# Optimization experiments

Hardware: AMD Instinct MI355X
Metric: run time of the kernel (lower is better)

Reference implementation:

```python
import jax, jax.numpy as jnp
import numpy as np

HEADS = 8
HEAD_DIM = 64
FOLD = 2   # fold_w == fold_h
PROP = 2   # proposal_w == proposal_h -> M = PROP*PROP centers
DIM = 512


def _conv1x1(x, w, b):
    # x: [B,C,H,W], w: [O,C] (1x1 conv kernel squeezed), b: [O]
    return jnp.einsum('bchw,oc->bohw', x, w) + b[None, :, None, None]


def _normalize(x):
    # F.normalize along last dim (eps-clamped L2 norm)
    n = jnp.linalg.norm(x, axis=-1, keepdims=True)
    return x / jnp.maximum(n, 1e-12)


def _fold(t, f):
    # 'b c (f1 w) (f2 h) -> (b f1 f2) c w h'
    b, c, W, H = t.shape
    return t.reshape(b, c, f, W // f, f, H // f).transpose(0, 2, 4, 1, 3, 5).reshape(b * f * f, c, W // f, H // f)


def _unfold(t, f):
    # '(b f1 f2) c w h -> b c (f1 w) (f2 h)'
    bf, c, w, h = t.shape
    b = bf // (f * f)
    return t.reshape(b, f, f, c, w, h).transpose(0, 3, 1, 4, 2, 5).reshape(b, c, f * w, f * h)


def _pool(t, p):
    # AdaptiveAvgPool2d((p,p)) when spatial dims divisible by p
    b, c, W, H = t.shape
    return t.reshape(b, c, p, W // p, p, H // p).mean(axis=(3, 5))


def reference(x, f_w, f_b, v_w, v_b, proj_w, proj_b, sim_alpha, sim_beta):
    B = x.shape[0]
    value = _conv1x1(x, v_w, v_b)
    feat = _conv1x1(x, f_w, f_b)
    # split heads: 'b (e c) w h -> (b e) c w h'
    feat = feat.reshape(B * HEADS, HEAD_DIM, feat.shape[2], feat.shape[3])
    value = value.reshape(B * HEADS, HEAD_DIM, value.shape[2], value.shape[3])
    feat = _fold(feat, FOLD)
    value = _fold(value, FOLD)
    b, c, w, h = feat.shape

    centers = _pool(feat, PROP)                                   # [b,c,p,p]
    value_centers = _pool(value, PROP).reshape(b, c, -1).transpose(0, 2, 1)  # [b,M,c]
    cflat = centers.reshape(b, c, -1).transpose(0, 2, 1)          # [b,M,c]
    M = cflat.shape[1]
    xflat = feat.reshape(b, c, -1).transpose(0, 2, 1)             # [b,N,c]

    cos = jnp.einsum('bmc,bnc->bmn', _normalize(cflat), _normalize(xflat))
    sim = jax.nn.sigmoid(sim_beta + sim_alpha * cos)              # [b,M,N]

    idx = jnp.argmax(sim, axis=1)                                 # [b,N] hard assignment
    sim_max = jnp.max(sim, axis=1)
    L_Clst = -jnp.mean(sim_max)
    mask = jax.nn.one_hot(idx, M, dtype=sim.dtype).transpose(0, 2, 1)  # [b,M,N]
    L_Sep = jnp.mean(jnp.max(sim * (1.0 - mask), axis=1))
    Cn = _normalize(cflat)
    G = jnp.einsum('bmc,bkc->bmk', Cn, Cn)
    L_Orth = jnp.mean((G - jnp.eye(M, dtype=G.dtype)) ** 2)

    sim_m = sim * mask
    vflat = value.reshape(b, c, -1).transpose(0, 2, 1)            # [b,N,c]
    # scatter_sum of values into their assigned cluster == one-hot matmul
    agg = jnp.einsum('bmn,bnc->bmc', mask, vflat)                 # [b,M,c]
    counts = mask.sum(axis=-1, keepdims=True)                     # [b,M,1]
    out = (agg + value_centers) / (counts + 1.0)                  # [b,M,c]
    # masked weighted broadcast back to points (avoids [b,M,N,c] intermediate)
    outp = jnp.einsum('bmn,bmc->bnc', sim_m, out)                 # [b,N,c]
    outp = outp.transpose(0, 2, 1).reshape(b, c, w, h)
    outp = _unfold(outp, FOLD)
    outp = outp.reshape(B, HEADS * HEAD_DIM, outp.shape[2], outp.shape[3])
    outp = _conv1x1(outp, proj_w, proj_b)
    return outp, jnp.stack([L_Orth, L_Clst, L_Sep])


def setup_inputs():
    key = jax.random.key(0)
    ks = jax.random.split(key, 4)
    E = HEADS * HEAD_DIM  # 512
    return {
        'x': jax.random.normal(ks[0], (32, DIM, 32, 32), jnp.float32),
        'f_w': jax.random.normal(ks[1], (E, DIM), jnp.float32) * 0.02,
        'f_b': jnp.zeros((E,), jnp.float32),
        'v_w': jax.random.normal(ks[2], (E, DIM), jnp.float32) * 0.02,
        'v_b': jnp.zeros((E,), jnp.float32),
        'proj_w': jax.random.normal(ks[3], (DIM, E), jnp.float32) * 0.02,
        'proj_b': jnp.zeros((DIM,), jnp.float32),
        'sim_alpha': jnp.ones((1,), jnp.float32),
        'sim_beta': jnp.zeros((1,), jnp.float32),
    }
```

## Files before the change

### kernel.cpp

```cpp
#include <hip/hip_runtime.h>


#define HW 1024

typedef _Float16 f16x8 __attribute__((ext_vector_type(8)));
typedef float f32x4 __attribute__((ext_vector_type(4)));

union H4 { uint2 u; _Float16 h[4]; };
union H8 { uint4 u; _Float16 h[8]; };
union H2 { unsigned int u; _Float16 h[2]; };
union F4 { float4 v; float f[4]; };

__device__ __forceinline__ void gld16(const _Float16* g, _Float16* l) {
    __builtin_amdgcn_global_load_lds(
        (const __attribute__((address_space(1))) void*)g,
        (__attribute__((address_space(3))) void*)l, 16, 0, 0);
}

__global__ __launch_bounds__(256) void k_wsplit(
    const float* __restrict__ fw, const float* __restrict__ vw,
    _Float16* __restrict__ fwh, _Float16* __restrict__ fwl,
    _Float16* __restrict__ vwh)
{
    const int i = (blockIdx.x * 256 + threadIdx.x) * 4;
    F4 a;
    a.v = *(const float4*)&fw[i];
    H4 h, l;
#pragma unroll
    for (int j = 0; j < 4; ++j) {
        const float s = a.f[j] * 256.f;
        h.h[j] = (_Float16)s;
        l.h[j] = (_Float16)(s - (float)h.h[j]);
    }
    *(uint2*)&fwh[i] = h.u;
    *(uint2*)&fwl[i] = l.u;
    a.v = *(const float4*)&vw[i];
#pragma unroll
    for (int j = 0; j < 4; ++j) h.h[j] = (_Float16)(a.f[j] * 256.f);
    *(uint2*)&vwh[i] = h.u;
}

__global__ __launch_bounds__(256) void k_xsplit(
    const float* __restrict__ x,
    _Float16* __restrict__ xh, _Float16* __restrict__ xl)
{
    __shared__ float tile[64][65];
    const int t = threadIdx.x;
    const int b = blockIdx.z;
    const int k0 = blockIdx.y * 64;
    const int n0 = blockIdx.x * 64;
    const float* Xb = x + (size_t)b * (512 * HW);

#pragma unroll
    for (int j = 0; j < 16; ++j) {
        const int k = j * 4 + (t >> 6);
        const int n = t & 63;
        tile[k][n] = Xb[(size_t)(k0 + k) * HW + n0 + n];
    }
    __syncthreads();
#pragma unroll
    for (int j = 0; j < 8; ++j) {
        const int n = j * 8 + (t >> 5);
        const int kp = t & 31;
        const float s0 = tile[kp * 2][n] * 256.f;
        const float s1 = tile[kp * 2 + 1][n] * 256.f;
        H2 hh, hl;
        hh.h[0] = (_Float16)s0;
        hh.h[1] = (_Float16)s1;
        hl.h[0] = (_Float16)(s0 - (float)hh.h[0]);
        hl.h[1] = (_Float16)(s1 - (float)hh.h[1]);
        const size_t o = ((size_t)b * 1024 + n0 + n) * 512 + k0 + kp * 2;
        *(unsigned int*)&xh[o] = hh.u;
        *(unsigned int*)&xl[o] = hl.u;
    }
}

__global__ __launch_bounds__(512, 2) void k_featval(
    const _Float16* __restrict__ fwh, const _Float16* __restrict__ fwl,
    const _Float16* __restrict__ vwh,
    const float* __restrict__ f_b, const float* __restrict__ v_b,
    const _Float16* __restrict__ xh, const _Float16* __restrict__ xl,
    float* __restrict__ feat_T, float* __restrict__ centers_f,
    _Float16* __restrict__ value_T, float* __restrict__ centers_v)
{
    __shared__ _Float16 Ah[2][8192], Al[2][8192], Bh[2][8192], Bl[2][8192];
    __shared__ float pool_lds[4][4][256];
    const int t = threadIdx.x, lane = t & 63, wv = t >> 6;
    const int b = blockIdx.z, o0 = blockIdx.y * 256, p0 = blockIdx.x * 256;
    const int wr = wv >> 2, wc = wv & 3;

    f32x4 acc[8][4];
#pragma unroll
    for (int i = 0; i < 8; ++i)
#pragma unroll
        for (int j = 0; j < 4; ++j) acc[i][j] = (f32x4){0.f, 0.f, 0.f, 0.f};

    const int gslot = ((lane & 3) ^ ((lane >> 3) & 3)) * 8;
    const _Float16* ash = fwh + (size_t)(o0 + wv * 32 + (lane >> 2)) * 512 + gslot;
    const _Float16* asl = fwl + (size_t)(o0 + wv * 32 + (lane >> 2)) * 512 + gslot;
    const _Float16* asv = vwh + (size_t)(o0 + wv * 32 + (lane >> 2)) * 512 + gslot;
    const size_t brow = (size_t)b * 1024 + p0 + wv * 32 + (lane >> 2);
    const _Float16* bsh = xh + brow * 512 + gslot;
    const _Float16* bsl = xl + brow * 512 + gslot;

#define STAGE_F(d, k0)                                              \
    {                                                               \
        gld16(ash + (k0),        &Ah[(d)][(wv * 32) * 32]);         \
        gld16(ash + (k0) + 8192, &Ah[(d)][(wv * 32 + 16) * 32]);    \
        gld16(asl + (k0),        &Al[(d)][(wv * 32) * 32]);         \
        gld16(asl + (k0) + 8192, &Al[(d)][(wv * 32 + 16) * 32]);    \
        gld16(bsh + (k0),        &Bh[(d)][(wv * 32) * 32]);         \
        gld16(bsh + (k0) + 8192, &Bh[(d)][(wv * 32 + 16) * 32]);    \
        gld16(bsl + (k0),        &Bl[(d)][(wv * 32) * 32]);         \
        gld16(bsl + (k0) + 8192, &Bl[(d)][(wv * 32 + 16) * 32]);    \
    }
#define STAGE_W(d, k0)                                              \
    {                                                               \
        gld16(asv + (k0),        &Ah[(d)][(wv * 32) * 32]);         \
        gld16(asv + (k0) + 8192, &Ah[(d)][(wv * 32 + 16) * 32]);    \
        gld16(bsh + (k0),        &Bh[(d)][(wv * 32) * 32]);         \
        gld16(bsh + (k0) + 8192, &Bh[(d)][(wv * 32 + 16) * 32]);    \
    }

    STAGE_F(0, 0);
    const int slA = ((lane >> 4) ^ ((lane >> 1) & 3)) * 8;
    int cur = 0;
    for (int kb = 0; kb < 16; ++kb) {
        if (kb < 15) {
            STAGE_F(cur ^ 1, (kb + 1) * 32);
            asm volatile("s_waitcnt vmcnt(8)" ::: "memory");
        } else {
            asm volatile("s_waitcnt vmcnt(0)" ::: "memory");
        }
        __builtin_amdgcn_sched_barrier(0);
        __builtin_amdgcn_s_barrier();
        f16x8 bh4[4], bl4[4];
#pragma unroll
        for (int j = 0; j < 4; ++j) {
            const int bo = (wc * 64 + j * 16 + (lane & 15)) * 32 + slA;
            bh4[j] = *(f16x8*)&Bh[cur][bo];
            bl4[j] = *(f16x8*)&Bl[cur][bo];
        }
#pragma unroll
        for (int mi = 0; mi < 8; ++mi) {
            const int ao = (wr * 128 + mi * 16 + (lane & 15)) * 32 + slA;
            const f16x8 ah = *(f16x8*)&Ah[cur][ao];
            const f16x8 al = *(f16x8*)&Al[cur][ao];
#pragma unroll
            for (int nj = 0; nj < 4; ++nj) {
                acc[mi][nj] = __builtin_amdgcn_mfma_f32_16x16x32_f16(ah, bh4[nj], acc[mi][nj], 0, 0, 0);
                acc[mi][nj] = __builtin_amdgcn_mfma_f32_16x16x32_f16(ah, bl4[nj], acc[mi][nj], 0, 0, 0);
                acc[mi][nj] = __builtin_amdgcn_mfma_f32_16x16x32_f16(al, bh4[nj], acc[mi][nj], 0, 0, 0);
            }
        }
        __builtin_amdgcn_s_barrier();
        cur ^= 1;
    }

    STAGE_W(0, 0);

    const int pj = (lane >> 3) & 1;
    {
        float ps[32][2];
#pragma unroll
        for (int mi = 0; mi < 8; ++mi) {
            const int obase = o0 + wr * 128 + mi * 16 + (lane >> 4) * 4;
            F4 bs4;
            bs4.v = *(const float4*)&f_b[obase];
#pragma unroll
            for (int r = 0; r < 4; ++r) { ps[mi * 4 + r][0] = 0.f; ps[mi * 4 + r][1] = 0.f; }
#pragma unroll
            for (int nj = 0; nj < 4; ++nj) {
                const int p = p0 + wc * 64 + nj * 16 + (lane & 15);
                F4 vv;
#pragma unroll
                for (int r = 0; r < 4; ++r) {
                    vv.f[r] = acc[mi][nj][r] * (1.f / 65536.f) + bs4.f[r];
                    ps[mi * 4 + r][nj & 1] += vv.f[r];
                }
                *(float4*)&feat_T[((size_t)b * 1024 + p) * 512 + obase] = vv.v;
            }
        }
#pragma unroll
        for (int q = 0; q < 32; ++q)
#pragma unroll
            for (int f2s = 0; f2s < 2; ++f2s) {
                ps[q][f2s] += __shfl_xor(ps[q][f2s], 1);
                ps[q][f2s] += __shfl_xor(ps[q][f2s], 2);
                ps[q][f2s] += __shfl_xor(ps[q][f2s], 4);
            }
        if ((lane & 7) == 0) {
#pragma unroll
            for (int mi = 0; mi < 8; ++mi)
#pragma unroll
                for (int r = 0; r < 4; ++r) {
                    const int ol = wr * 128 + mi * 16 + (lane >> 4) * 4 + r;
                    pool_lds[wc][0 * 2 + pj][ol] = ps[mi * 4 + r][0];
                    pool_lds[wc][1 * 2 + pj][ol] = ps[mi * 4 + r][1];
                }
        }
        __syncthreads();
#pragma unroll
        for (int u = 0; u < 2; ++u) {
            const int idx = u * 512 + t;
            const int g = idx >> 8, o = idx & 255;
            const float s = pool_lds[0][g][o] + pool_lds[1][g][o]
                          + pool_lds[2][g][o] + pool_lds[3][g][o];
            centers_f[(((size_t)b * 8 + 2 * blockIdx.x) * 4 + g) * 512 + o0 + o] = s;
            centers_f[(((size_t)b * 8 + 2 * blockIdx.x + 1) * 4 + g) * 512 + o0 + o] = 0.f;
        }
    }

    f32x4 vacc[8][4];
#pragma unroll
    for (int i = 0; i < 8; ++i)
#pragma unroll
        for (int j = 0; j < 4; ++j) vacc[i][j] = (f32x4){0.f, 0.f, 0.f, 0.f};

    cur = 0;
    for (int kb = 0; kb < 16; ++kb) {
        if (kb < 15) {
            STAGE_W(cur ^ 1, (kb + 1) * 32);
            asm volatile("s_waitcnt vmcnt(4)" ::: "memory");
        } else {
            asm volatile("s_waitcnt vmcnt(0)" ::: "memory");
        }
        __builtin_amdgcn_sched_barrier(0);
        __builtin_amdgcn_s_barrier();
        f16x8 bh4[4];
#pragma unroll
        for (int j = 0; j < 4; ++j)
            bh4[j] = *(f16x8*)&Bh[cur][(wc * 64 + j * 16 + (lane & 15)) * 32 + slA];
#pragma unroll
        for (int mi = 0; mi < 8; ++mi) {
            const f16x8 ah = *(f16x8*)&Ah[cur][(wr * 128 + mi * 16 + (lane & 15)) * 32 + slA];
#pragma unroll
            for (int nj = 0; nj < 4; ++nj)
                vacc[mi][nj] = __builtin_amdgcn_mfma_f32_16x16x32_f16(ah, bh4[nj], vacc[mi][nj], 0, 0, 0);
        }
        __builtin_amdgcn_s_barrier();
        cur ^= 1;
    }
#undef STAGE_F
#undef STAGE_W

    {
        float ps[32][2];
#pragma unroll
        for (int mi = 0; mi < 8; ++mi) {
            const int obase = o0 + wr * 128 + mi * 16 + (lane >> 4) * 4;
            F4 bs4;
            bs4.v = *(const float4*)&v_b[obase];
#pragma unroll
            for (int r = 0; r < 4; ++r) { ps[mi * 4 + r][0] = 0.f; ps[mi * 4 + r][1] = 0.f; }
#pragma unroll
            for (int nj = 0; nj < 4; ++nj) {
                const int p = p0 + wc * 64 + nj * 16 + (lane & 15);
                H4 hv;
#pragma unroll
                for (int r = 0; r < 4; ++r) {
                    const float v = vacc[mi][nj][r] * (1.f / 65536.f) + bs4.f[r];
                    ps[mi * 4 + r][nj & 1] += v;
                    hv.h[r] = (_Float16)v;
                }
                *(uint2*)&value_T[((size_t)b * 1024 + p) * 512 + obase] = hv.u;
            }
        }
#pragma unroll
        for (int q = 0; q < 32; ++q)
#pragma unroll
            for (int f2s = 0; f2s < 2; ++f2s) {
                ps[q][f2s] += __shfl_xor(ps[q][f2s], 1);
                ps[q][f2s] += __shfl_xor(ps[q][f2s], 2);
                ps[q][f2s] += __shfl_xor(ps[q][f2s], 4);
            }
        __syncthreads();
        if ((lane & 7) == 0) {
#pragma unroll
            for (int mi = 0; mi < 8; ++mi)
#pragma unroll
                for (int r = 0; r < 4; ++r) {
                    const int ol = wr * 128 + mi * 16 + (lane >> 4) * 4 + r;
                    pool_lds[wc][0 * 2 + pj][ol] = ps[mi * 4 + r][0];
                    pool_lds[wc][1 * 2 + pj][ol] = ps[mi * 4 + r][1];
                }
        }
        __syncthreads();
#pragma unroll
        for (int u = 0; u < 2; ++u) {
            const int idx = u * 512 + t;
            const int g = idx >> 8, o = idx & 255;
            const float s = pool_lds[0][g][o] + pool_lds[1][g][o]
                          + pool_lds[2][g][o] + pool_lds[3][g][o];
            centers_v[(((size_t)b * 8 + 2 * blockIdx.x) * 4 + g) * 512 + o0 + o] = s;
            centers_v[(((size_t)b * 8 + 2 * blockIdx.x + 1) * 4 + g) * 512 + o0 + o] = 0.f;
        }
    }
}

__global__ __launch_bounds__(256) void k_cluster(
    const float* __restrict__ feat_T, const _Float16* __restrict__ value_T,
    const float* __restrict__ centers_f, const float* __restrict__ centers_v,
    const float* __restrict__ alpha_p, const float* __restrict__ beta_p,
    _Float16* __restrict__ outpT, float* __restrict__ part)
{
    __shared__ float cnl[4][64];
    __shared__ float vcl[4][64];
    __shared__ float obuf[4][68];
    __shared__ int   sidx[256];
    __shared__ float sbest[256];
    __shared__ float scrt[4][4][64];
    __shared__ int   cntw[4][4];
    __shared__ float red[8];
    __shared__ float gsc[16];

    const int t = threadIdx.x, lane = t & 63, wv = t >> 6;
    const int bp = blockIdx.x;
    const int f2 = bp & 1, f1 = (bp >> 1) & 1, head = (bp >> 2) & 7, b = bp >> 5;

    const int m = wv, cc = lane;
    const int pi = m >> 1, pj = m & 1, g = f2 * 2 + pj;
    const int pt = 4 * f1 + 2 * pi;
    {
        const float* cf = centers_f + (((size_t)b * 8 + pt) * 4 + g) * 512 + head * 64 + cc;
        const float c = (cf[0] + cf[4 * 512]) * (1.f / 64.f);
        float ss = c * c;
#pragma unroll
        for (int off = 32; off > 0; off >>= 1) ss += __shfl_xor(ss, off);
        const float inv = 1.f / fmaxf(sqrtf(ss), 1e-12f);
        cnl[m][cc] = c * inv;
        const float* cv = centers_v + (((size_t)b * 8 + pt) * 4 + g) * 512 + head * 64 + cc;
        vcl[m][cc] = (cv[0] + cv[4 * 512]) * (1.f / 64.f);
    }
    __syncthreads();

    if (t < 16) {
        const int gm = t >> 2, gk = t & 3;
        float gg = 0.f;
        for (int c = 0; c < 64; ++c) gg += cnl[gm][c] * cnl[gk][c];
        const float d = gg - (gm == gk ? 1.f : 0.f);
        gsc[t] = d * d;
    }

    const float alpha = alpha_p[0], beta = beta_p[0];
    const int n = t;
    const int pg = (f1 * 16 + (n >> 4)) * 32 + f2 * 16 + (n & 15);
    const float* fp = feat_T + ((size_t)b * 1024 + pg) * 512 + head * 64;
    float ssf = 0.f, d0 = 0.f, d1 = 0.f, d2 = 0.f, d3 = 0.f;
#pragma unroll
    for (int c4 = 0; c4 < 16; ++c4) {
        F4 fv;
        fv.v = *(const float4*)&fp[c4 * 4];
        const float4 c0 = *(const float4*)&cnl[0][c4 * 4];
        const float4 c1 = *(const float4*)&cnl[1][c4 * 4];
        const float4 c2 = *(const float4*)&cnl[2][c4 * 4];
        const float4 c3 = *(const float4*)&cnl[3][c4 * 4];
        ssf += fv.f[0]*fv.f[0] + fv.f[1]*fv.f[1] + fv.f[2]*fv.f[2] + fv.f[3]*fv.f[3];
        d0 += fv.f[0]*c0.x + fv.f[1]*c0.y + fv.f[2]*c0.z + fv.f[3]*c0.w;
        d1 += fv.f[0]*c1.x + fv.f[1]*c1.y + fv.f[2]*c1.z + fv.f[3]*c1.w;
        d2 += fv.f[0]*c2.x + fv.f[1]*c2.y + fv.f[2]*c2.z + fv.f[3]*c2.w;
        d3 += fv.f[0]*c3.x + fv.f[1]*c3.y + fv.f[2]*c3.z + fv.f[3]*c3.w;
    }
    const float invf = 1.f / fmaxf(sqrtf(ssf), 1e-12f);
    float simv[4];
    simv[0] = d0 * invf;
    simv[1] = d1 * invf;
    simv[2] = d2 * invf;
    simv[3] = d3 * invf;
#pragma unroll
    for (int mm = 0; mm < 4; ++mm)
        simv[mm] = 1.f / (1.f + expf(-(beta + alpha * simv[mm])));
    float best = simv[0], second = -1.f;
    int idx = 0;
#pragma unroll
    for (int mm = 1; mm < 4; ++mm) {
        if (simv[mm] > best) { second = best; best = simv[mm]; idx = mm; }
        else second = fmaxf(second, simv[mm]);
    }
    sidx[n] = idx;
    sbest[n] = best;

    float bsum = best, s2sum = second;
#pragma unroll
    for (int off = 32; off > 0; off >>= 1) {
        bsum += __shfl_xor(bsum, off);
        s2sum += __shfl_xor(s2sum, off);
    }
    if (lane == 0) { red[wv] = bsum; red[4 + wv] = s2sum; }
    __syncthreads();
    if (t == 0) {
        part[bp]        = gsc[0] + gsc[1] + gsc[2] + gsc[3] + gsc[4] + gsc[5] + gsc[6] + gsc[7]
                        + gsc[8] + gsc[9] + gsc[10] + gsc[11] + gsc[12] + gsc[13] + gsc[14] + gsc[15];
        part[1024 + bp] = red[0] + red[1] + red[2] + red[3];
        part[2048 + bp] = red[4] + red[5] + red[6] + red[7];
    }

    {
        const _Float16* vT = value_T + ((size_t)b * 1024) * 512 + head * 64 + cc;
        const int rowbase = (f1 * 16 + wv * 4) * 32 + f2 * 16;
        float ag0 = 0.f, ag1 = 0.f, ag2 = 0.f, ag3 = 0.f;
        int c0i = 0, c1i = 0, c2i = 0, c3i = 0;
#pragma unroll 8
        for (int j = 0; j < 64; ++j) {
            const int nn = wv * 64 + j;
            const int id = sidx[nn];
            const int pgn = rowbase + (j >> 4) * 32 + (j & 15);
            const float v = (float)vT[(size_t)pgn * 512];
            ag0 += (id == 0) ? v : 0.f;  c0i += (id == 0);
            ag1 += (id == 1) ? v : 0.f;  c1i += (id == 1);
            ag2 += (id == 2) ? v : 0.f;  c2i += (id == 2);
            ag3 += (id == 3) ? v : 0.f;  c3i += (id == 3);
        }
        scrt[wv][0][cc] = ag0;
        scrt[wv][1][cc] = ag1;
        scrt[wv][2][cc] = ag2;
        scrt[wv][3][cc] = ag3;
        if (lane == 0) {
            cntw[wv][0] = c0i; cntw[wv][1] = c1i;
            cntw[wv][2] = c2i; cntw[wv][3] = c3i;
        }
    }
    __syncthreads();

    {
        const float a = scrt[0][m][cc] + scrt[1][m][cc] + scrt[2][m][cc] + scrt[3][m][cc];
        const int c = cntw[0][m] + cntw[1][m] + cntw[2][m] + cntw[3][m];
        obuf[m][cc] = (a + vcl[m][cc]) / (float)(c + 1);
    }
    __syncthreads();

    const int cch = (t & 3) * 16;
#pragma unroll
    for (int r = 0; r < 4; ++r) {
        const int nn = r * 64 + (t >> 2);
        const int id = sidx[nn];
        const float bs = sbest[nn];
        const int p = (f1 * 16 + (nn >> 4)) * 32 + f2 * 16 + (nn & 15);
        _Float16* dst = outpT + (((size_t)b * 8 + head) * 1024 + p) * 64 + cch;
        const float4 oa = *(const float4*)&obuf[id][cch];
        const float4 ob = *(const float4*)&obuf[id][cch + 4];
        const float4 oc = *(const float4*)&obuf[id][cch + 8];
        const float4 od = *(const float4*)&obuf[id][cch + 12];
        H8 w0, w1;
        w0.h[0] = (_Float16)(bs * oa.x); w0.h[1] = (_Float16)(bs * oa.y);
        w0.h[2] = (_Float16)(bs * oa.z); w0.h[3] = (_Float16)(bs * oa.w);
        w0.h[4] = (_Float16)(bs * ob.x); w0.h[5] = (_Float16)(bs * ob.y);
        w0.h[6] = (_Float16)(bs * ob.z); w0.h[7] = (_Float16)(bs * ob.w);
        w1.h[0] = (_Float16)(bs * oc.x); w1.h[1] = (_Float16)(bs * oc.y);
        w1.h[2] = (_Float16)(bs * oc.z); w1.h[3] = (_Float16)(bs * oc.w);
        w1.h[4] = (_Float16)(bs * od.x); w1.h[5] = (_Float16)(bs * od.y);
        w1.h[6] = (_Float16)(bs * od.z); w1.h[7] = (_Float16)(bs * od.w);
        *(uint4*)dst = w0.u;
        *(uint4*)(dst + 8) = w1.u;
    }
}

__global__ __launch_bounds__(256) void k_proj(
    const float* __restrict__ w, const float* __restrict__ bias,
    const _Float16* __restrict__ outpT,
    const float* __restrict__ part,
    float* __restrict__ dout)
{
    __shared__ _Float16 As[2][4096], Bs[2][4096];
    __shared__ float fin[12];
    const int t = threadIdx.x, lane = t & 63, wv = t >> 6;

    if (blockIdx.x == 0 && blockIdx.y == 0 && blockIdx.z == 0) {
        float so = part[t] + part[t + 256] + part[t + 512] + part[t + 768];
        float sc = part[1024 + t] + part[1280 + t] + part[1536 + t] + part[1792 + t];
        float sp = part[2048 + t] + part[2304 + t] + part[2560 + t] + part[2816 + t];
#pragma unroll
        for (int off = 32; off > 0; off >>= 1) {
            so += __shfl_xor(so, off);
            sc += __shfl_xor(sc, off);
            sp += __shfl_xor(sp, off);
        }
        if (lane == 0) { fin[wv] = so; fin[4 + wv] = sc; fin[8 + wv] = sp; }
        __syncthreads();
        if (t == 0) {
            dout[16777216]     = (fin[0] + fin[1] + fin[2] + fin[3]) / 16384.f;
            dout[16777216 + 1] = -(fin[4] + fin[5] + fin[6] + fin[7]) / 262144.f;
            dout[16777216 + 2] = (fin[8] + fin[9] + fin[10] + fin[11]) / 262144.f;
        }
        __syncthreads();
    }

    const int b = blockIdx.z, o0 = blockIdx.y * 128, p0 = blockIdx.x * 128;
    const int wr = wv >> 1, wc = wv & 1;

    f32x4 acc[4][4];
#pragma unroll
    for (int i = 0; i < 4; ++i)
#pragma unroll
        for (int j = 0; j < 4; ++j) acc[i][j] = (f32x4){0.f, 0.f, 0.f, 0.f};

    const int gslot = ((lane & 3) ^ ((lane >> 3) & 3)) * 8;
    const int srow = p0 + wv * 32 + (lane >> 2);
    const int arow_l = t >> 3;
    const int aq = t & 7;
    const int aqs = aq ^ (((t >> 4) & 3) << 1);

    F4 av[4];
#define LOADA(k0)                                                        \
    {                                                                    \
        _Pragma("unroll")                                                \
        for (int j = 0; j < 4; ++j)                                      \
            av[j].v = *(const float4*)&w[(size_t)(o0 + j * 32 + arow_l) * 512 + (k0) + aq * 4]; \
    }
#define WRITEA(d)                                                        \
    {                                                                    \
        _Pragma("unroll")                                                \
        for (int j = 0; j < 4; ++j) {                                    \
            H4 hh;                                                       \
            _Pragma("unroll")                                            \
            for (int i = 0; i < 4; ++i) hh.h[i] = (_Float16)(av[j].f[i] * 256.f); \
            *(uint2*)&As[(d)][(j * 32 + arow_l) * 32 + aqs * 4] = hh.u;  \
        }                                                                \
    }
#define STAGEB(d, kb)                                                    \
    {                                                                    \
        const _Float16* bsrc = outpT + (((size_t)b * 8 + ((kb) >> 1)) * 1024 + srow) * 64 \
                               + ((kb) & 1) * 32 + gslot;                \
        gld16(bsrc,        &Bs[(d)][(wv * 32) * 32]);                    \
        gld16(bsrc + 1024, &Bs[(d)][(wv * 32 + 16) * 32]);               \
    }

    LOADA(0);
    STAGEB(0, 0);
    WRITEA(0);
    __syncthreads();
    const int slA = ((lane >> 4) ^ ((lane >> 1) & 3)) * 8;
    int cur = 0;
    for (int kb = 0; kb < 16; ++kb) {
        if (kb < 15) {
            LOADA((kb + 1) * 32);
            STAGEB(cur ^ 1, kb + 1);
        }
        f16x8 ah4[4], bh4[4];
#pragma unroll
        for (int i = 0; i < 4; ++i) {
            ah4[i] = *(f16x8*)&As[cur][(wr * 64 + i * 16 + (lane & 15)) * 32 + slA];
            bh4[i] = *(f16x8*)&Bs[cur][(wc * 64 + i * 16 + (lane & 15)) * 32 + slA];
        }
#pragma unroll
        for (int mi = 0; mi < 4; ++mi)
#pragma unroll
            for (int nj = 0; nj < 4; ++nj)
                acc[mi][nj] = __builtin_amdgcn_mfma_f32_16x16x32_f16(ah4[mi], bh4[nj], acc[mi][nj], 0, 0, 0);
        if (kb < 15) WRITEA(cur ^ 1);
        __syncthreads();
        cur ^= 1;
    }
#undef LOADA
#undef WRITEA
#undef STAGEB

#pragma unroll
    for (int mi = 0; mi < 4; ++mi)
#pragma unroll
        for (int r = 0; r < 4; ++r) {
            const int o = o0 + wr * 64 + mi * 16 + (lane >> 4) * 4 + r;
            const float bs = bias[o];
#pragma unroll
            for (int nj = 0; nj < 4; ++nj) {
                const int p = p0 + wc * 64 + nj * 16 + (lane & 15);
                dout[((size_t)b * 512 + o) * HW + p] = acc[mi][nj][r] * (1.f / 256.f) + bs;
            }
        }
}

extern "C" void kernel_launch(void* const* d_in, const int* in_sizes, int n_in,
                              void* d_out, int out_size, void* d_ws, size_t ws_size,
                              hipStream_t stream)
{
    const float* x   = (const float*)d_in[0];
    const float* f_w = (const float*)d_in[1];
    const float* f_b = (const float*)d_in[2];
    const float* v_w = (const float*)d_in[3];
    const float* v_b = (const float*)d_in[4];
    const float* p_w = (const float*)d_in[5];
    const float* p_b = (const float*)d_in[6];
    const float* s_a = (const float*)d_in[7];
    const float* s_b = (const float*)d_in[8];
    float* out = (float*)d_out;

    char* ws = (char*)d_ws;
    float*     feat_T  = (float*)ws;
    _Float16*  xh      = (_Float16*)(ws + (size_t)64 * 1024 * 1024);
    _Float16*  xl      = (_Float16*)(ws + (size_t)96 * 1024 * 1024);
    _Float16*  outpT   = xh;
    _Float16*  value_T = xl;
    float*     part    = (float*)(ws + (size_t)128 * 1024 * 1024);

    _Float16* fwh       = (_Float16*)out;
    _Float16* fwl       = (_Float16*)(out + 131072);
    _Float16* vwh       = (_Float16*)(out + 262144);
    float*    centers_f = out + 524288;
    float*    centers_v = out + 1048576;

    k_wsplit <<<dim3(256), 256, 0, stream>>>(f_w, v_w, fwh, fwl, vwh);
    k_xsplit <<<dim3(16, 8, 32), 256, 0, stream>>>(x, xh, xl);
    k_featval<<<dim3(4, 2, 32), 512, 0, stream>>>(fwh, fwl, vwh, f_b, v_b, xh, xl,
                                                  feat_T, centers_f, value_T, centers_v);
    k_cluster<<<dim3(1024), 256, 0, stream>>>(feat_T, value_T, centers_f, centers_v,
                                              s_a, s_b, outpT, part);
    k_proj   <<<dim3(8, 4, 32), 256, 0, stream>>>(p_w, p_b, outpT, part, out);
}
```

Before: 186.0 us.

## Fold weight split into x-split kernel and enlarge proj tile to 256x256

Removes the separate weight-split launch by having batch-0 blocks of the x-split kernel also convert f_w/v_w to fp16 hi/lo. The projection GEMM moves from 128x128 tiles with 4 waves to 256x256 tiles with 8 waves. This gives more operand reuse per LDS load, with A fragments loaded per row-tile inside the MFMA loop. __syncthreads is replaced by explicit vmcnt/lgkmcnt waits and s_barrier so global loads overlap compute. Larger tiles cut the grid to 256 blocks and raise register/LDS pressure, and the hand-written wait counts risk races if miscounted.

```diff
diff --git a/kernel.cpp b/kernel.cpp
--- a/kernel.cpp
+++ b/kernel.cpp
@@ -17,40 +17,43 @@
         (__attribute__((address_space(3))) void*)l, 16, 0, 0);
 }
 
-__global__ __launch_bounds__(256) void k_wsplit(
+__global__ __launch_bounds__(256) void k_xsplit(
+    const float* __restrict__ x,
+    _Float16* __restrict__ xh, _Float16* __restrict__ xl,
     const float* __restrict__ fw, const float* __restrict__ vw,
     _Float16* __restrict__ fwh, _Float16* __restrict__ fwl,
     _Float16* __restrict__ vwh)
-{
-    const int i = (blockIdx.x * 256 + threadIdx.x) * 4;
-    F4 a;
-    a.v = *(const float4*)&fw[i];
-    H4 h, l;
-#pragma unroll
-    for (int j = 0; j < 4; ++j) {
-        const float s = a.f[j] * 256.f;
-        h.h[j] = (_Float16)s;
-        l.h[j] = (_Float16)(s - (float)h.h[j]);
-    }
-    *(uint2*)&fwh[i] = h.u;
-    *(uint2*)&fwl[i] = l.u;
-    a.v = *(const float4*)&vw[i];
-#pragma unroll
-    for (int j = 0; j < 4; ++j) h.h[j] = (_Float16)(a.f[j] * 256.f);
-    *(uint2*)&vwh[i] = h.u;
-}
-
-__global__ __launch_bounds__(256) void k_xsplit(
-    const float* __restrict__ x,
-    _Float16* __restrict__ xh, _Float16* __restrict__ xl)
 {
     __shared__ float tile[64][65];
     const int t = threadIdx.x;
     const int b = blockIdx.z;
     const int k0 = blockIdx.y * 64;
     const int n0 = blockIdx.x * 64;
+
+    if (b == 0) {
+        const int c0 = (blockIdx.x * 8 + blockIdx.y) * 2;
+#pragma unroll
+        for (int u = 0; u < 2; ++u) {
+            const int i = ((c0 + u) * 256 + t) * 4;
+            F4 a;
+            a.v = *(const float4*)&fw[i];
+            H4 h, l;
+#pragma unroll
+            for (int j = 0; j < 4; ++j) {
+                const float s = a.f[j] * 256.f;
+                h.h[j] = (_Float16)s;
+                l.h[j] = (_Float16)(s - (float)h.h[j]);
+            }
+            *(uint2*)&fwh[i] = h.u;
+            *(uint2*)&fwl[i] = l.u;
+            a.v = *(const float4*)&vw[i];
+#pragma unroll
+            for (int j = 0; j < 4; ++j) h.h[j] = (_Float16)(a.f[j] * 256.f);
+            *(uint2*)&vwh[i] = h.u;
+        }
+    }
+
     const float* Xb = x + (size_t)b * (512 * HW);
-
 #pragma unroll
     for (int j = 0; j < 16; ++j) {
         const int k = j * 4 + (t >> 6);
@@ -455,48 +458,51 @@
     }
 }
 
-__global__ __launch_bounds__(256) void k_proj(
+__global__ __launch_bounds__(512, 2) void k_proj(
     const float* __restrict__ w, const float* __restrict__ bias,
     const _Float16* __restrict__ outpT,
     const float* __restrict__ part,
     float* __restrict__ dout)
 {
-    __shared__ _Float16 As[2][4096], Bs[2][4096];
-    __shared__ float fin[12];
+    __shared__ _Float16 As[2][8192], Bs[2][8192];
+    __shared__ float fin[24];
     const int t = threadIdx.x, lane = t & 63, wv = t >> 6;
 
     if (blockIdx.x == 0 && blockIdx.y == 0 && blockIdx.z == 0) {
-        float so = part[t] + part[t + 256] + part[t + 512] + part[t + 768];
-        float sc = part[1024 + t] + part[1280 + t] + part[1536 + t] + part[1792 + t];
-        float sp = part[2048 + t] + part[2304 + t] + part[2560 + t] + part[2816 + t];
+        float so = part[t] + part[t + 512];
+        float sc = part[1024 + t] + part[1536 + t];
+        float sp = part[2048 + t] + part[2560 + t];
 #pragma unroll
         for (int off = 32; off > 0; off >>= 1) {
             so += __shfl_xor(so, off);
             sc += __shfl_xor(sc, off);
             sp += __shfl_xor(sp, off);
         }
-        if (lane == 0) { fin[wv] = so; fin[4 + wv] = sc; fin[8 + wv] = sp; }
+        if (lane == 0) { fin[wv] = so; fin[8 + wv] = sc; fin[16 + wv] = sp; }
         __syncthreads();
         if (t == 0) {
-            dout[16777216]     = (fin[0] + fin[1] + fin[2] + fin[3]) / 16384.f;
-            dout[16777216 + 1] = -(fin[4] + fin[5] + fin[6] + fin[7]) / 262144.f;
-            dout[16777216 + 2] = (fin[8] + fin[9] + fin[10] + fin[11]) / 262144.f;
+            float a = 0.f, bsum = 0.f, c = 0.f;
+#pragma unroll
+            for (int i = 0; i < 8; ++i) { a += fin[i]; bsum += fin[8 + i]; c += fin[16 + i]; }
+            dout[16777216]     = a / 16384.f;
+            dout[16777216 + 1] = -bsum / 262144.f;
+            dout[16777216 + 2] = c / 262144.f;
         }
         __syncthreads();
     }
 
-    const int b = blockIdx.z, o0 = blockIdx.y * 128, p0 = blockIdx.x * 128;
-    const int wr = wv >> 1, wc = wv & 1;
-
-    f32x4 acc[4][4];
-#pragma unroll
-    for (int i = 0; i < 4; ++i)
+    const int b = blockIdx.z, o0 = blockIdx.y * 256, p0 = blockIdx.x * 256;
+    const int wr = wv >> 2, wc = wv & 3;
+
+    f32x4 acc[8][4];
+#pragma unroll
+    for (int i = 0; i < 8; ++i)
 #pragma unroll
         for (int j = 0; j < 4; ++j) acc[i][j] = (f32x4){0.f, 0.f, 0.f, 0.f};
 
     const int gslot = ((lane & 3) ^ ((lane >> 3) & 3)) * 8;
     const int srow = p0 + wv * 32 + (lane >> 2);
-    const int arow_l = t >> 3;
+    const int arow = t >> 3;
     const int aq = t & 7;
     const int aqs = aq ^ (((t >> 4) & 3) << 1);
 
@@ -505,7 +511,7 @@
     {                                                                    \
         _Pragma("unroll")                                                \
         for (int j = 0; j < 4; ++j)                                      \
-            av[j].v = *(const float4*)&w[(size_t)(o0 + j * 32 + arow_l) * 512 + (k0) + aq * 4]; \
+            av[j].v = *(const float4*)&w[(size_t)(o0 + j * 64 + arow) * 512 + (k0) + aq * 4]; \
     }
 #define WRITEA(d)                                                        \
     {                                                                    \
@@ -514,7 +520,7 @@
             H4 hh;                                                       \
             _Pragma("unroll")                                            \
             for (int i = 0; i < 4; ++i) hh.h[i] = (_Float16)(av[j].f[i] * 256.f); \
-            *(uint2*)&As[(d)][(j * 32 + arow_l) * 32 + aqs * 4] = hh.u;  \
+            *(uint2*)&As[(d)][(j * 64 + arow) * 32 + aqs * 4] = hh.u;    \
         }                                                                \
     }
 #define STAGEB(d, kb)                                                    \
@@ -528,27 +534,37 @@
     LOADA(0);
     STAGEB(0, 0);
     WRITEA(0);
-    __syncthreads();
+    asm volatile("s_waitcnt lgkmcnt(0)" ::: "memory");
     const int slA = ((lane >> 4) ^ ((lane >> 1) & 3)) * 8;
     int cur = 0;
     for (int kb = 0; kb < 16; ++kb) {
         if (kb < 15) {
             LOADA((kb + 1) * 32);
             STAGEB(cur ^ 1, kb + 1);
-        }
-        f16x8 ah4[4], bh4[4];
-#pragma unroll
-        for (int i = 0; i < 4; ++i) {
-            ah4[i] = *(f16x8*)&As[cur][(wr * 64 + i * 16 + (lane & 15)) * 32 + slA];
-            bh4[i] = *(f16x8*)&Bs[cur][(wc * 64 + i * 16 + (lane & 15)) * 32 + slA];
-        }
-#pragma unroll
-        for (int mi = 0; mi < 4; ++mi)
+            asm volatile("s_waitcnt vmcnt(6)" ::: "memory");
+        } else {
+            asm volatile("s_waitcnt vmcnt(0)" ::: "memory");
+        }
+        __builtin_amdgcn_sched_barrier(0);
+        __builtin_amdgcn_s_barrier();
+        f16x8 bh4[4];
+#pragma unroll
+        for (int j = 0; j < 4; ++j)
+            bh4[j] = *(f16x8*)&Bs[cur][(wc * 64 + j * 16 + (lane & 15)) * 32 + slA];
+#pragma unroll
+        for (int mi = 0; mi < 8; ++mi) {
+            const f16x8 ah = *(f16x8*)&As[cur][(wr * 128 + mi * 16 + (lane & 15)) * 32 + slA];
 #pragma unroll
             for (int nj = 0; nj < 4; ++nj)
-                acc[mi][nj] = __builtin_amdgcn_mfma_f32_16x16x32_f16(ah4[mi], bh4[nj], acc[mi][nj], 0, 0, 0);
-        if (kb < 15) WRITEA(cur ^ 1);
-        __syncthreads();
+                acc[mi][nj] = __builtin_amdgcn_mfma_f32_16x16x32_f16(ah, bh4[nj], acc[mi][nj], 0, 0, 0);
+        }
+        if (kb < 15) {
+            asm volatile("s_waitcnt vmcnt(2)" ::: "memory");
+            __builtin_amdgcn_sched_barrier(0);
+            WRITEA(cur ^ 1);
+        }
+        asm volatile("s_waitcnt lgkmcnt(0)" ::: "memory");
+        __builtin_amdgcn_s_barrier();
         cur ^= 1;
     }
 #undef LOADA
@@ -556,10 +572,10 @@
 #undef STAGEB
 
 #pragma unroll
-    for (int mi = 0; mi < 4; ++mi)
+    for (int mi = 0; mi < 8; ++mi)
 #pragma unroll
         for (int r = 0; r < 4; ++r) {
-            const int o = o0 + wr * 64 + mi * 16 + (lane >> 4) * 4 + r;
+            const int o = o0 + wr * 128 + mi * 16 + (lane >> 4) * 4 + r;
             const float bs = bias[o];
 #pragma unroll
             for (int nj = 0; nj < 4; ++nj) {
@@ -598,11 +614,10 @@
     float*    centers_f = out + 524288;
     float*    centers_v = out + 1048576;
 
-    k_wsplit <<<dim3(256), 256, 0, stream>>>(f_w, v_w, fwh, fwl, vwh);
-    k_xsplit <<<dim3(16, 8, 32), 256, 0, stream>>>(x, xh, xl);
+    k_xsplit <<<dim3(16, 8, 32), 256, 0, stream>>>(x, xh, xl, f_w, v_w, fwh, fwl, vwh);
     k_featval<<<dim3(4, 2, 32), 512, 0, stream>>>(fwh, fwl, vwh, f_b, v_b, xh, xl,
                                                   feat_T, centers_f, value_T, centers_v);
     k_cluster<<<dim3(1024), 256, 0, stream>>>(feat_T, value_T, centers_f, centers_v,
                                               s_a, s_b, outpT, part);
-    k_proj   <<<dim3(8, 4, 32), 256, 0, stream>>>(p_w, p_b, outpT, part, out);
+    k_proj   <<<dim3(4, 2, 32), 512, 0, stream>>>(p_w, p_b, outpT, part, out);
 }
```

Measured after the change: 190.4 us. +2.3%, slower.

## Fuse weight split into x split and remap block order for L2 locality

Applied to the files above, without the earlier changes.

Folds the weight fp16 split kernel into the batch-0 blocks of the x split kernel, which removes one launch. It also flattens the featval and proj grids to 1D with a custom block-index mapping, so blocks scheduled close together (likely across the XCDs) share weight tiles or batch data in cache. The cost is extra index arithmetic and some imbalance, since batch-0 blocks of the split kernel do more work.

```diff
diff --git a/kernel.cpp b/kernel.cpp
--- a/kernel.cpp
+++ b/kernel.cpp
@@ -17,40 +17,43 @@
         (__attribute__((address_space(3))) void*)l, 16, 0, 0);
 }
 
-__global__ __launch_bounds__(256) void k_wsplit(
+__global__ __launch_bounds__(256) void k_xsplit(
+    const float* __restrict__ x,
+    _Float16* __restrict__ xh, _Float16* __restrict__ xl,
     const float* __restrict__ fw, const float* __restrict__ vw,
     _Float16* __restrict__ fwh, _Float16* __restrict__ fwl,
     _Float16* __restrict__ vwh)
-{
-    const int i = (blockIdx.x * 256 + threadIdx.x) * 4;
-    F4 a;
-    a.v = *(const float4*)&fw[i];
-    H4 h, l;
-#pragma unroll
-    for (int j = 0; j < 4; ++j) {
-        const float s = a.f[j] * 256.f;
-        h.h[j] = (_Float16)s;
-        l.h[j] = (_Float16)(s - (float)h.h[j]);
-    }
-    *(uint2*)&fwh[i] = h.u;
-    *(uint2*)&fwl[i] = l.u;
-    a.v = *(const float4*)&vw[i];
-#pragma unroll
-    for (int j = 0; j < 4; ++j) h.h[j] = (_Float16)(a.f[j] * 256.f);
-    *(uint2*)&vwh[i] = h.u;
-}
-
-__global__ __launch_bounds__(256) void k_xsplit(
-    const float* __restrict__ x,
-    _Float16* __restrict__ xh, _Float16* __restrict__ xl)
 {
     __shared__ float tile[64][65];
     const int t = threadIdx.x;
     const int b = blockIdx.z;
     const int k0 = blockIdx.y * 64;
     const int n0 = blockIdx.x * 64;
+
+    if (b == 0) {
+        const int c0 = (blockIdx.x * 8 + blockIdx.y) * 2;
+#pragma unroll
+        for (int u = 0; u < 2; ++u) {
+            const int i = ((c0 + u) * 256 + t) * 4;
+            F4 a;
+            a.v = *(const float4*)&fw[i];
+            H4 h, l;
+#pragma unroll
+            for (int j = 0; j < 4; ++j) {
+                const float s = a.f[j] * 256.f;
+                h.h[j] = (_Float16)s;
+                l.h[j] = (_Float16)(s - (float)h.h[j]);
+            }
+            *(uint2*)&fwh[i] = h.u;
+            *(uint2*)&fwl[i] = l.u;
+            a.v = *(const float4*)&vw[i];
+#pragma unroll
+            for (int j = 0; j < 4; ++j) h.h[j] = (_Float16)(a.f[j] * 256.f);
+            *(uint2*)&vwh[i] = h.u;
+        }
+    }
+
     const float* Xb = x + (size_t)b * (512 * HW);
-
 #pragma unroll
     for (int j = 0; j < 16; ++j) {
         const int k = j * 4 + (t >> 6);
@@ -86,7 +89,14 @@
     __shared__ _Float16 Ah[2][8192], Al[2][8192], Bh[2][8192], Bl[2][8192];
     __shared__ float pool_lds[4][4][256];
     const int t = threadIdx.x, lane = t & 63, wv = t >> 6;
-    const int b = blockIdx.z, o0 = blockIdx.y * 256, p0 = blockIdx.x * 256;
+
+    const int bid = blockIdx.x;
+    const int r_ = bid & 15, u_ = bid >> 4;
+    const int yy = r_ >> 3;
+    const int v_ = u_ * 8 + (r_ & 7);
+    const int xx = v_ & 3, zz = v_ >> 2;
+
+    const int b = zz, o0 = yy * 256, p0 = xx * 256;
     const int wr = wv >> 2, wc = wv & 3;
 
     f32x4 acc[8][4];
@@ -206,8 +216,8 @@
             const int g = idx >> 8, o = idx & 255;
             const float s = pool_lds[0][g][o] + pool_lds[1][g][o]
                           + pool_lds[2][g][o] + pool_lds[3][g][o];
-            centers_f[(((size_t)b * 8 + 2 * blockIdx.x) * 4 + g) * 512 + o0 + o] = s;
-            centers_f[(((size_t)b * 8 + 2 * blockIdx.x + 1) * 4 + g) * 512 + o0 + o] = 0.f;
+            centers_f[(((size_t)b * 8 + 2 * xx) * 4 + g) * 512 + o0 + o] = s;
+            centers_f[(((size_t)b * 8 + 2 * xx + 1) * 4 + g) * 512 + o0 + o] = 0.f;
         }
     }
 
@@ -292,8 +302,8 @@
             const int g = idx >> 8, o = idx & 255;
             const float s = pool_lds[0][g][o] + pool_lds[1][g][o]
                           + pool_lds[2][g][o] + pool_lds[3][g][o];
-            centers_v[(((size_t)b * 8 + 2 * blockIdx.x) * 4 + g) * 512 + o0 + o] = s;
-            centers_v[(((size_t)b * 8 + 2 * blockIdx.x + 1) * 4 + g) * 512 + o0 + o] = 0.f;
+            centers_v[(((size_t)b * 8 + 2 * xx) * 4 + g) * 512 + o0 + o] = s;
+            centers_v[(((size_t)b * 8 + 2 * xx + 1) * 4 + g) * 512 + o0 + o] = 0.f;
         }
     }
 }
@@ -465,7 +475,13 @@
     __shared__ float fin[12];
     const int t = threadIdx.x, lane = t & 63, wv = t >> 6;
 
-    if (blockIdx.x == 0 && blockIdx.y == 0 && blockIdx.z == 0) {
+    const int bid = blockIdx.x;
+    const int r_ = bid & 31;
+    const int yy = r_ >> 3;
+    const int v_ = (bid >> 5) * 8 + (r_ & 7);
+    const int xx = v_ & 7, zz = v_ >> 3;
+
+    if (bid == 0) {
         float so = part[t] + part[t + 256] + part[t + 512] + part[t + 768];
         float sc = part[1024 + t] + part[1280 + t] + part[1536 + t] + part[1792 + t];
         float sp = part[2048 + t] + part[2304 + t] + part[2560 + t] + part[2816 + t];
@@ -485,7 +501,7 @@
         __syncthreads();
     }
 
-    const int b = blockIdx.z, o0 = blockIdx.y * 128, p0 = blockIdx.x * 128;
+    const int b = zz, o0 = yy * 128, p0 = xx * 128;
     const int wr = wv >> 1, wc = wv & 1;
 
     f32x4 acc[4][4];
@@ -598,11 +614,10 @@
     float*    centers_f = out + 524288;
     float*    centers_v = out + 1048576;
 
-    k_wsplit <<<dim3(256), 256, 0, stream>>>(f_w, v_w, fwh, fwl, vwh);
-    k_xsplit <<<dim3(16, 8, 32), 256, 0, stream>>>(x, xh, xl);
-    k_featval<<<dim3(4, 2, 32), 512, 0, stream>>>(fwh, fwl, vwh, f_b, v_b, xh, xl,
-                                                  feat_T, centers_f, value_T, centers_v);
+    k_xsplit <<<dim3(16, 8, 32), 256, 0, stream>>>(x, xh, xl, f_w, v_w, fwh, fwl, vwh);
+    k_featval<<<dim3(256), 512, 0, stream>>>(fwh, fwl, vwh, f_b, v_b, xh, xl,
+                                             feat_T, centers_f, value_T, centers_v);
     k_cluster<<<dim3(1024), 256, 0, stream>>>(feat_T, value_T, centers_f, centers_v,
                                               s_a, s_b, outpT, part);
-    k_proj   <<<dim3(8, 4, 32), 256, 0, stream>>>(p_w, p_b, outpT, part, out);
+    k_proj   <<<dim3(1024), 256, 0, stream>>>(p_w, p_b, outpT, part, out);
 }
```

Result: faster. 180.0 us (-3.2%).
